# Kernel tuning notes

Measured on AMD Instinct MI355X. Metric: run time of the kernel, lower is better.

The kernel has to match this reference:

```python
import jax, jax.numpy as jnp
import numpy as np

H, DH = 16, 64  # heads, dim_head; inner = H*DH = 1024
EPS = 1e-5


def _ln(t, g, b):
    mu = jnp.mean(t, axis=-1, keepdims=True)
    var = jnp.var(t, axis=-1, keepdims=True)
    return (t - mu) * jax.lax.rsqrt(var + EPS) * g + b


def _split_heads(t):
    b, n, _ = t.shape
    return t.reshape(b, n, H, DH).transpose(0, 2, 1, 3)  # (b,h,n,dh)


def setup_inputs() -> dict:
    key = jax.random.key(0)
    ks = jax.random.split(key, 5)
    B, S, M, D = 16, 64, 4096, 1024  # S must equal DH (see source einsum quirk)
    return {
        "x": jax.random.normal(ks[0], (B, S, D), jnp.float32),
        "latents": jax.random.normal(ks[1], (B, M, D), jnp.float32),
        "ln_x_g": jnp.ones((D,), jnp.float32),
        "ln_x_b": jnp.zeros((D,), jnp.float32),
        "ln_l_g": jnp.ones((D,), jnp.float32),
        "ln_l_b": jnp.zeros((D,), jnp.float32),
        "Wq": jax.random.normal(ks[2], (D, H * DH), jnp.float32) * 0.02,
        "Wkv": jax.random.normal(ks[3], (D, 2 * H * DH), jnp.float32) * 0.02,
        "Wout": jax.random.normal(ks[4], (H * DH, D), jnp.float32) * 0.02,
    }


def reference(x, latents, ln_x_g, ln_x_b, ln_l_g, ln_l_b, Wq, Wkv, Wout):
    scale = DH ** -0.5
    xn = _ln(x, ln_x_g, ln_x_b)          # (B,S,D)
    ln = _ln(latents, ln_l_g, ln_l_b)    # (B,M,D)
    q = _split_heads(ln @ Wq) * scale    # (B,H,M,DH)
    k, v = map(_split_heads, jnp.split(xn @ Wkv, 2, axis=-1))  # (B,H,S,DH)
    sim = jnp.einsum('bhid,bhjd->bhij', q, k)                  # (B,H,M,S)
    sim = sim - jax.lax.stop_gradient(jnp.max(sim, axis=-1, keepdims=True))
    attn = jax.nn.softmax(sim, axis=-1)
    # Faithful to source: einsum('b h i d, b h j d -> b h i j', attn, v)
    # contracts attn's S dim with v's DH dim (requires S == DH); out = attn @ v^T.
    out = jnp.einsum('bhis,bhjs->bhij', attn, v)               # (B,H,M,S)
    b, _, m, _ = out.shape
    out = out.transpose(0, 2, 1, 3).reshape(b, m, H * DH)      # (B,M,inner)
    return out @ Wout                                          # (B,M,D)
```

## Files before the change

### kernel.cpp

```cpp
#include <hip/hip_runtime.h>
#include <stdint.h>

#define B_ 16
#define S_ 64
#define M_ 4096
#define D_ 1024
#define H_ 16
#define DH_ 64

typedef unsigned short ushort_t;
typedef __attribute__((ext_vector_type(8))) __bf16 bfrag;
typedef __attribute__((ext_vector_type(4))) float f32x4;

__device__ __forceinline__ ushort_t f2bf(float f) {
  union { float f; uint32_t u; } v; v.f = f;
  uint32_t r = v.u + 0x7fffu + ((v.u >> 16) & 1u);
  return (ushort_t)(r >> 16);
}

__device__ __forceinline__ void gload_lds16(const void* g, void* l) {
  __builtin_amdgcn_global_load_lds((const __attribute__((address_space(1))) void*)g,
                                   (__attribute__((address_space(3))) void*)l, 16, 0, 0);
}

__device__ __forceinline__ f32x4 mfma16x16x32(bfrag a, bfrag b, f32x4 c) {
  return __builtin_amdgcn_mfma_f32_16x16x32_bf16(a, b, c, 0, 0, 0);
}

__device__ __forceinline__ int fsw(int r) { return (((r >> 2) & 3) << 1) | (r & 1); }

__global__ __launch_bounds__(256) void ln_rows_kernel(
    const float* __restrict__ x, const float* __restrict__ g,
    const float* __restrict__ bta, ushort_t* __restrict__ out) {
  const int row = blockIdx.x;
  const int t = threadIdx.x;
  const float4* xr = (const float4*)(x + (size_t)row * D_);
  float4 v = xr[t];
  float s = v.x + v.y + v.z + v.w;
  float ss = v.x * v.x + v.y * v.y + v.z * v.z + v.w * v.w;
#pragma unroll
  for (int o = 32; o >= 1; o >>= 1) { s += __shfl_down(s, o); ss += __shfl_down(ss, o); }
  __shared__ float red[16];
  const int wid = t >> 6;
  if ((t & 63) == 0) { red[wid] = s; red[8 + wid] = ss; }
  __syncthreads();
  float tot = red[0] + red[1] + red[2] + red[3];
  float tot2 = red[8] + red[9] + red[10] + red[11];
  float mu = tot * (1.0f / D_);
  float var = tot2 * (1.0f / D_) - mu * mu;
  float rstd = rsqrtf(var + 1e-5f);
  float4 gg = ((const float4*)g)[t];
  float4 bb = ((const float4*)bta)[t];
  ushort_t ob[4];
  ob[0] = f2bf((v.x - mu) * rstd * gg.x + bb.x);
  ob[1] = f2bf((v.y - mu) * rstd * gg.y + bb.y);
  ob[2] = f2bf((v.z - mu) * rstd * gg.z + bb.z);
  ob[3] = f2bf((v.w - mu) * rstd * gg.w + bb.w);
  *(uint2*)(out + (size_t)row * D_ + t * 4) = *(const uint2*)ob;
}

__global__ void transpose_cast_kernel(const float* __restrict__ W, ushort_t* __restrict__ WT,
                                      int N, float scale) {
  __shared__ float tile[32][33];
  const int n0 = blockIdx.x * 32, k0 = blockIdx.y * 32;
  const int tx = threadIdx.x, ty = threadIdx.y;
#pragma unroll
  for (int i = ty; i < 32; i += 8)
    tile[i][tx] = W[(size_t)(k0 + i) * N + n0 + tx];
  __syncthreads();
#pragma unroll
  for (int i = ty; i < 32; i += 8)
    WT[(size_t)(n0 + i) * D_ + k0 + tx] = f2bf(tile[tx][i] * scale);
}

__global__ __launch_bounds__(256) void gemm_kv_kernel(
    const ushort_t* __restrict__ A, const ushort_t* __restrict__ Bt,
    ushort_t* __restrict__ kb, ushort_t* __restrict__ vb) {
  __shared__ __align__(16) ushort_t sA[128 * 32];
  __shared__ __align__(16) ushort_t sB[128 * 32];
  const int tid = threadIdx.x, wid = tid >> 6, lane = tid & 63;
  const size_t arow0 = (size_t)blockIdx.x * 128;
  const size_t brow0 = (size_t)blockIdx.y * 128;
  const int wr = (wid >> 1) * 64, wc = (wid & 1) * 64;
  const int srow = tid >> 2, scol = (tid & 3) * 8;
  const ushort_t* ga = A + (arow0 + srow) * (size_t)D_ + scol;
  const ushort_t* gb = Bt + (brow0 + srow) * (size_t)D_ + scol;
  const int frow = lane & 15, kslot = (lane >> 4) * 8;
  f32x4 acc[4][4] = {};
  for (int k0 = 0; k0 < D_; k0 += 32) {
    gload_lds16(ga, sA + wid * 512);
    gload_lds16(ga + 64 * (size_t)D_, sA + 2048 + wid * 512);
    gload_lds16(gb, sB + wid * 512);
    gload_lds16(gb + 64 * (size_t)D_, sB + 2048 + wid * 512);
    ga += 32; gb += 32;
    __syncthreads();
    bfrag af[4], bfv[4];
#pragma unroll
    for (int m = 0; m < 4; ++m)
      af[m] = *(const bfrag*)&sA[(wr + m * 16 + frow) * 32 + kslot];
#pragma unroll
    for (int n = 0; n < 4; ++n)
      bfv[n] = *(const bfrag*)&sB[(wc + n * 16 + frow) * 32 + kslot];
#pragma unroll
    for (int m = 0; m < 4; ++m)
#pragma unroll
      for (int n = 0; n < 4; ++n)
        acc[m][n] = mfma16x16x32(af[m], bfv[n], acc[m][n]);
    __syncthreads();
  }
  const int erow = (lane >> 4) * 4, ecol = lane & 15;
#pragma unroll
  for (int m = 0; m < 4; ++m)
#pragma unroll
    for (int n = 0; n < 4; ++n)
#pragma unroll
      for (int r = 0; r < 4; ++r) {
        size_t i = arow0 + wr + m * 16 + erow + r;
        int bb = (int)(i >> 6), s = (int)(i & 63);
        size_t n2 = brow0 + wc + n * 16 + ecol;
        ushort_t val = f2bf(acc[m][n][r]);
        ushort_t* dst = (n2 < 1024) ? kb : vb;
        size_t hh = (n2 & 1023) >> 6, d = n2 & 63;
        dst[(((size_t)bb * H_ + hh) * S_ + s) * DH_ + d] = val;
      }
}

template <int MODE>
__global__ __launch_bounds__(512, 2) void gemm256_kernel(
    const ushort_t* __restrict__ A, const ushort_t* __restrict__ Bt,
    const ushort_t* __restrict__ kbuf, const ushort_t* __restrict__ vbuf,
    void* __restrict__ Cout) {
  __shared__ __align__(16) ushort_t lds[32768];
  const int tid = threadIdx.x, wid = tid >> 6, lane = tid & 63;
  const int frow = lane & 15, klo = lane >> 4;
  const int wm = wid >> 2, wn = wid & 3;

  const int l = ((int)blockIdx.x & 7) * 128 + ((int)blockIdx.x >> 3);
  const int mblk = l >> 2, nblk = l & 3;
  const size_t arow0 = (size_t)mblk * 256;
  const size_t bcol0 = (size_t)nblk * 256;

  const int srow = tid >> 3;
  const int sgsw = tid & 7;
  const int G = sgsw ^ (srow & 7);
  const int side = G >> 2, g2 = G & 3;
  const ushort_t* pA = A + (arow0 + (size_t)(side * 128 + srow)) * D_ + g2 * 8;
  const ushort_t* pB = Bt + (bcol0 + (size_t)((side * 2 + (srow >> 5)) * 64 + (srow & 31))) * D_ + g2 * 8;

  gload_lds16(pB, &lds[16384 + wid * 512]);
  gload_lds16(pB + 32 * D_, &lds[16384 + 4096 + wid * 512]);
  gload_lds16(pA, &lds[wid * 512]);
  gload_lds16(pA + 64 * D_, &lds[4096 + wid * 512]);

  f32x4 acc[8][4] = {};
  for (int kt = 0; kt < 32; ++kt) {
    const int d = kt & 1, nd = d ^ 1;
    const int kn = (kt < 31 ? kt + 1 : 31) * 32;
    bfrag ar[4], br[4];
    gload_lds16(pB + kn, &lds[16384 + nd * 8192 + wid * 512]);
    gload_lds16(pB + 32 * D_ + kn, &lds[16384 + nd * 8192 + 4096 + wid * 512]);
    asm volatile("s_waitcnt vmcnt(3)" ::: "memory");
    __builtin_amdgcn_s_barrier();
    __builtin_amdgcn_sched_barrier(0);
#pragma unroll
    for (int mf2 = 0; mf2 < 4; ++mf2) {
      const int i = mf2 * 16 + frow;
      const int gsw = (wm * 4 + klo) ^ (i & 7);
      ar[mf2] = *(const bfrag*)&lds[d * 8192 + i * 64 + gsw * 8];
    }
#pragma unroll
    for (int nf = 0; nf < 4; ++nf) {
      const int p1 = nf >> 1;
      const int t = (wn & 1) * 32 + (nf & 1) * 16 + frow;
      const int gsw = ((wn >> 1) * 4 + klo) ^ (t & 7);
      br[nf] = *(const bfrag*)&lds[16384 + d * 8192 + p1 * 4096 + t * 64 + gsw * 8];
    }
    __builtin_amdgcn_s_setprio(1);
#pragma unroll
    for (int mf2 = 0; mf2 < 4; ++mf2)
#pragma unroll
      for (int nf = 0; nf < 4; ++nf)
        acc[mf2][nf] = mfma16x16x32(ar[mf2], br[nf], acc[mf2][nf]);
    __builtin_amdgcn_s_setprio(0);
    gload_lds16(pA + kn, &lds[nd * 8192 + wid * 512]);
    gload_lds16(pA + 64 * D_ + kn, &lds[nd * 8192 + 4096 + wid * 512]);
    asm volatile("s_waitcnt vmcnt(4)" ::: "memory");
    __builtin_amdgcn_s_barrier();
    __builtin_amdgcn_sched_barrier(0);
#pragma unroll
    for (int mf2 = 0; mf2 < 4; ++mf2) {
      const int i = mf2 * 16 + frow;
      const int gsw = (wm * 4 + klo) ^ (i & 7);
      ar[mf2] = *(const bfrag*)&lds[d * 8192 + 4096 + i * 64 + gsw * 8];
    }
    __builtin_amdgcn_s_setprio(1);
#pragma unroll
    for (int mf2 = 0; mf2 < 4; ++mf2)
#pragma unroll
      for (int nf = 0; nf < 4; ++nf)
        acc[4 + mf2][nf] = mfma16x16x32(ar[mf2], br[nf], acc[4 + mf2][nf]);
    __builtin_amdgcn_s_setprio(0);
    __builtin_amdgcn_s_barrier();
  }
  asm volatile("s_waitcnt vmcnt(0)" ::: "memory");
  __builtin_amdgcn_s_barrier();
  __builtin_amdgcn_sched_barrier(0);

  if constexpr (MODE == 0) {
    float* C = (float*)Cout;
#pragma unroll
    for (int m = 0; m < 8; ++m)
#pragma unroll
      for (int n = 0; n < 4; ++n)
#pragma unroll
        for (int r = 0; r < 4; ++r)
          C[(arow0 + wm * 128 + m * 16 + klo * 4 + r) * 1024 + bcol0 + wn * 64 + n * 16 + frow] =
              acc[m][n][r];
  } else {
    ushort_t* W = &lds[wid * 4096];
    ushort_t* out1 = (ushort_t*)Cout;
    const int head = nblk * 4 + wn;
    const int bbatch = mblk >> 4;
    const size_t kvbase = ((size_t)bbatch * H_ + head) * (size_t)(S_ * DH_);
    bfrag kb[4][2], vb[4][2];
#pragma unroll
    for (int nf = 0; nf < 4; ++nf)
#pragma unroll
      for (int kk = 0; kk < 2; ++kk) {
        kb[nf][kk] = *(const bfrag*)&kbuf[kvbase + (nf * 16 + frow) * 64 + kk * 32 + klo * 8];
        vb[nf][kk] = *(const bfrag*)&vbuf[kvbase + (nf * 16 + frow) * 64 + kk * 32 + klo * 8];
      }
#pragma unroll
    for (int hh = 0; hh < 2; ++hh) {
#pragma unroll
      for (int m2 = 0; m2 < 4; ++m2)
#pragma unroll
        for (int r = 0; r < 4; ++r) {
          const int row = m2 * 16 + klo * 4 + r;
          const int fs = fsw(row);
#pragma unroll
          for (int n = 0; n < 4; ++n) {
            const int cc = n * 16 + frow;
            W[row * 64 + ((((cc >> 3) ^ fs) << 3) | (cc & 7))] = f2bf(acc[hh * 4 + m2][n][r]);
          }
        }
      f32x4 s[4][4] = {};
#pragma unroll
      for (int m2 = 0; m2 < 4; ++m2) {
        const int row = m2 * 16 + frow;
        const int fs = fsw(row);
#pragma unroll
        for (int kk = 0; kk < 2; ++kk) {
          bfrag qa = *(const bfrag*)&W[row * 64 + (((kk * 4 + klo) ^ fs) << 3)];
#pragma unroll
          for (int nf = 0; nf < 4; ++nf)
            s[m2][nf] = mfma16x16x32(qa, kb[nf][kk], s[m2][nf]);
        }
      }
#pragma unroll
      for (int m2 = 0; m2 < 4; ++m2)
#pragma unroll
        for (int r = 0; r < 4; ++r) {
          float a0 = s[m2][0][r], a1 = s[m2][1][r], a2 = s[m2][2][r], a3 = s[m2][3][r];
          float mx = fmaxf(fmaxf(a0, a1), fmaxf(a2, a3));
#pragma unroll
          for (int o = 1; o < 16; o <<= 1) mx = fmaxf(mx, __shfl_xor(mx, o));
          a0 = __expf(a0 - mx); a1 = __expf(a1 - mx);
          a2 = __expf(a2 - mx); a3 = __expf(a3 - mx);
          float sm = (a0 + a1) + (a2 + a3);
#pragma unroll
          for (int o = 1; o < 16; o <<= 1) sm += __shfl_xor(sm, o);
          const float inv = 1.0f / sm;
          s[m2][0][r] = a0 * inv; s[m2][1][r] = a1 * inv;
          s[m2][2][r] = a2 * inv; s[m2][3][r] = a3 * inv;
        }
#pragma unroll
      for (int m2 = 0; m2 < 4; ++m2)
#pragma unroll
        for (int r = 0; r < 4; ++r) {
          const int row = m2 * 16 + klo * 4 + r;
          const int fs = fsw(row);
#pragma unroll
          for (int n = 0; n < 4; ++n) {
            const int cc = n * 16 + frow;
            W[row * 64 + ((((cc >> 3) ^ fs) << 3) | (cc & 7))] = f2bf(s[m2][n][r]);
          }
        }
      f32x4 o[4][4] = {};
#pragma unroll
      for (int m2 = 0; m2 < 4; ++m2) {
        const int row = m2 * 16 + frow;
        const int fs = fsw(row);
#pragma unroll
        for (int kk = 0; kk < 2; ++kk) {
          bfrag pa = *(const bfrag*)&W[row * 64 + (((kk * 4 + klo) ^ fs) << 3)];
#pragma unroll
          for (int nf = 0; nf < 4; ++nf)
            o[m2][nf] = mfma16x16x32(pa, vb[nf][kk], o[m2][nf]);
        }
      }
#pragma unroll
      for (int m2 = 0; m2 < 4; ++m2)
#pragma unroll
        for (int r = 0; r < 4; ++r) {
          const int row = m2 * 16 + klo * 4 + r;
          const int fs = fsw(row);
#pragma unroll
          for (int n = 0; n < 4; ++n) {
            const int cc = n * 16 + frow;
            W[row * 64 + ((((cc >> 3) ^ fs) << 3) | (cc & 7))] = f2bf(o[m2][n][r]);
          }
        }
      const size_t grow0 = arow0 + wm * 128 + hh * 64;
#pragma unroll
      for (int it = 0; it < 8; ++it) {
        const int idx = it * 64 + lane;
        const int rr = idx >> 3, gs = idx & 7;
        const int gcol = (gs ^ fsw(rr)) << 3;
        *(uint4*)&out1[(grow0 + rr) * 1024 + head * 64 + gcol] =
            *(const uint4*)&W[rr * 64 + gs * 8];
      }
    }
  }
}

extern "C" void kernel_launch(void* const* d_in, const int* in_sizes, int n_in,
                              void* d_out, int out_size, void* d_ws, size_t ws_size,
                              hipStream_t stream) {
  const float* x = (const float*)d_in[0];
  const float* lat = (const float*)d_in[1];
  const float* lxg = (const float*)d_in[2];
  const float* lxb = (const float*)d_in[3];
  const float* llg = (const float*)d_in[4];
  const float* llb = (const float*)d_in[5];
  const float* Wq = (const float*)d_in[6];
  const float* Wkv = (const float*)d_in[7];
  const float* Wout = (const float*)d_in[8];
  float* out = (float*)d_out;
  char* ws = (char*)d_ws;

  ushort_t* xn = (ushort_t*)(ws);
  ushort_t* wqT = (ushort_t*)(ws + (2ull << 20));
  ushort_t* wkvT = (ushort_t*)(ws + (4ull << 20));
  ushort_t* woT = (ushort_t*)(ws + (8ull << 20));
  ushort_t* kbuf = (ushort_t*)(ws + (10ull << 20));
  ushort_t* vbuf = (ushort_t*)(ws + (12ull << 20));
  ushort_t* out1 = (ushort_t*)(ws + (14ull << 20));
  ushort_t* lnl = (ushort_t*)d_out;

  dim3 tb(32, 8);
  transpose_cast_kernel<<<dim3(1024 / 32, 32), tb, 0, stream>>>(Wq, wqT, 1024, 0.125f);
  transpose_cast_kernel<<<dim3(2048 / 32, 32), tb, 0, stream>>>(Wkv, wkvT, 2048, 1.0f);
  transpose_cast_kernel<<<dim3(1024 / 32, 32), tb, 0, stream>>>(Wout, woT, 1024, 1.0f);
  ln_rows_kernel<<<B_ * S_, 256, 0, stream>>>(x, lxg, lxb, xn);
  ln_rows_kernel<<<B_ * M_, 256, 0, stream>>>(lat, llg, llb, lnl);
  gemm_kv_kernel<<<dim3(8, 16), 256, 0, stream>>>(xn, wkvT, kbuf, vbuf);
  gemm256_kernel<1><<<1024, 512, 0, stream>>>(lnl, wqT, kbuf, vbuf, out1);
  gemm256_kernel<0><<<1024, 512, 0, stream>>>(out1, woT, nullptr, nullptr, out);
}
```

Before: 485.2 us.

## Deepen GEMM global-to-LDS pipeline to four stages with one barrier per k-step

The GEMM main loop moves from a two-slot LDS double buffer, with A and B halves loaded at staggered points, to a four-slot ring. Three k-tiles of A and B are prefetched ahead, so each iteration needs a single vmcnt wait and one barrier. All eight A fragments are read at once before the MFMAs. LDS per block doubles to 128 KB, which likely prevents two blocks per CU, and the tail iterations issue redundant clamped loads.

```diff
diff --git a/kernel.cpp b/kernel.cpp
--- a/kernel.cpp
+++ b/kernel.cpp
@@ -130,7 +130,7 @@
     const ushort_t* __restrict__ A, const ushort_t* __restrict__ Bt,
     const ushort_t* __restrict__ kbuf, const ushort_t* __restrict__ vbuf,
     void* __restrict__ Cout) {
-  __shared__ __align__(16) ushort_t lds[32768];
+  __shared__ __align__(16) ushort_t lds[65536];
   const int tid = threadIdx.x, wid = tid >> 6, lane = tid & 63;
   const int frow = lane & 15, klo = lane >> 4;
   const int wm = wid >> 2, wn = wid & 3;
@@ -147,64 +147,52 @@
   const ushort_t* pA = A + (arow0 + (size_t)(side * 128 + srow)) * D_ + g2 * 8;
   const ushort_t* pB = Bt + (bcol0 + (size_t)((side * 2 + (srow >> 5)) * 64 + (srow & 31))) * D_ + g2 * 8;
 
-  gload_lds16(pB, &lds[16384 + wid * 512]);
-  gload_lds16(pB + 32 * D_, &lds[16384 + 4096 + wid * 512]);
-  gload_lds16(pA, &lds[wid * 512]);
-  gload_lds16(pA + 64 * D_, &lds[4096 + wid * 512]);
+#define STAGE(KT)                                                                  \
+  do {                                                                             \
+    const int _s = (KT) & 3;                                                       \
+    const size_t _kn = (size_t)(((KT) < 32 ? (KT) : 31)) * 32;                     \
+    gload_lds16(pB + _kn, &lds[32768 + _s * 8192 + wid * 512]);                    \
+    gload_lds16(pB + 32 * (size_t)D_ + _kn, &lds[32768 + _s * 8192 + 4096 + wid * 512]); \
+    gload_lds16(pA + _kn, &lds[_s * 8192 + wid * 512]);                            \
+    gload_lds16(pA + 64 * (size_t)D_ + _kn, &lds[_s * 8192 + 4096 + wid * 512]);   \
+  } while (0)
+
+  STAGE(0);
+  STAGE(1);
+  STAGE(2);
 
   f32x4 acc[8][4] = {};
   for (int kt = 0; kt < 32; ++kt) {
-    const int d = kt & 1, nd = d ^ 1;
-    const int kn = (kt < 31 ? kt + 1 : 31) * 32;
-    bfrag ar[4], br[4];
-    gload_lds16(pB + kn, &lds[16384 + nd * 8192 + wid * 512]);
-    gload_lds16(pB + 32 * D_ + kn, &lds[16384 + nd * 8192 + 4096 + wid * 512]);
-    asm volatile("s_waitcnt vmcnt(3)" ::: "memory");
+    asm volatile("s_waitcnt vmcnt(8)" ::: "memory");
     __builtin_amdgcn_s_barrier();
     __builtin_amdgcn_sched_barrier(0);
-#pragma unroll
-    for (int mf2 = 0; mf2 < 4; ++mf2) {
-      const int i = mf2 * 16 + frow;
+    STAGE(kt + 3);
+    const int sl = kt & 3;
+    bfrag ar[8], br[4];
+#pragma unroll
+    for (int mf = 0; mf < 8; ++mf) {
+      const int i = (mf & 3) * 16 + frow;
       const int gsw = (wm * 4 + klo) ^ (i & 7);
-      ar[mf2] = *(const bfrag*)&lds[d * 8192 + i * 64 + gsw * 8];
+      ar[mf] = *(const bfrag*)&lds[sl * 8192 + (mf >> 2) * 4096 + i * 64 + gsw * 8];
     }
 #pragma unroll
     for (int nf = 0; nf < 4; ++nf) {
-      const int p1 = nf >> 1;
       const int t = (wn & 1) * 32 + (nf & 1) * 16 + frow;
       const int gsw = ((wn >> 1) * 4 + klo) ^ (t & 7);
-      br[nf] = *(const bfrag*)&lds[16384 + d * 8192 + p1 * 4096 + t * 64 + gsw * 8];
+      br[nf] = *(const bfrag*)&lds[32768 + sl * 8192 + (nf >> 1) * 4096 + t * 64 + gsw * 8];
     }
     __builtin_amdgcn_s_setprio(1);
 #pragma unroll
-    for (int mf2 = 0; mf2 < 4; ++mf2)
+    for (int mf = 0; mf < 8; ++mf)
 #pragma unroll
       for (int nf = 0; nf < 4; ++nf)
-        acc[mf2][nf] = mfma16x16x32(ar[mf2], br[nf], acc[mf2][nf]);
+        acc[mf][nf] = mfma16x16x32(ar[mf], br[nf], acc[mf][nf]);
     __builtin_amdgcn_s_setprio(0);
-    gload_lds16(pA + kn, &lds[nd * 8192 + wid * 512]);
-    gload_lds16(pA + 64 * D_ + kn, &lds[nd * 8192 + 4096 + wid * 512]);
-    asm volatile("s_waitcnt vmcnt(4)" ::: "memory");
-    __builtin_amdgcn_s_barrier();
-    __builtin_amdgcn_sched_barrier(0);
-#pragma unroll
-    for (int mf2 = 0; mf2 < 4; ++mf2) {
-      const int i = mf2 * 16 + frow;
-      const int gsw = (wm * 4 + klo) ^ (i & 7);
-      ar[mf2] = *(const bfrag*)&lds[d * 8192 + 4096 + i * 64 + gsw * 8];
-    }
-    __builtin_amdgcn_s_setprio(1);
-#pragma unroll
-    for (int mf2 = 0; mf2 < 4; ++mf2)
-#pragma unroll
-      for (int nf = 0; nf < 4; ++nf)
-        acc[4 + mf2][nf] = mfma16x16x32(ar[mf2], br[nf], acc[4 + mf2][nf]);
-    __builtin_amdgcn_s_setprio(0);
-    __builtin_amdgcn_s_barrier();
   }
   asm volatile("s_waitcnt vmcnt(0)" ::: "memory");
   __builtin_amdgcn_s_barrier();
   __builtin_amdgcn_sched_barrier(0);
+#undef STAGE
 
   if constexpr (MODE == 0) {
     float* C = (float*)Cout;
```

Result: no change. 477.1 us (-1.7%).
